# Kernel optimization log

Measured on AMD Instinct MI355X. Metric: run time of the kernel, lower is better.

Reference implementation:

```python
import jax, jax.numpy as jnp
import numpy as np

MASK_SIZE = 28

def _box_iou(a, b):
    # a: [P,4], b: [G,4] in (x1,y1,x2,y2) -> [P,G] IoU (torchvision box_iou semantics)
    area_a = (a[:, 2] - a[:, 0]) * (a[:, 3] - a[:, 1])
    area_b = (b[:, 2] - b[:, 0]) * (b[:, 3] - b[:, 1])
    lt = jnp.maximum(a[:, None, :2], b[None, :, :2])
    rb = jnp.minimum(a[:, None, 2:], b[None, :, 2:])
    wh = jnp.clip(rb - lt, 0.0)
    inter = wh[..., 0] * wh[..., 1]
    return inter / (area_a[:, None] + area_b[None, :] - inter)

def _extract_targets(gt_masks, midx, mboxes):
    # Vectorized equivalent of the per-box Python loop in extract_mask_target:
    # clamp int box, crop gt mask, bilinear-resize (align_corners=False) to 28x28.
    G, H, W = gt_masks.shape
    b = mboxes.astype(jnp.int32)  # .int() truncation; boxes are non-negative here
    x1 = jnp.clip(b[:, 0], 0, W - 1)
    y1 = jnp.clip(b[:, 1], 0, H - 1)
    x2 = jnp.maximum(x1 + 1, jnp.minimum(b[:, 2], W))
    y2 = jnp.maximum(y1 + 1, jnp.minimum(b[:, 3], H))
    cw = (x2 - x1).astype(jnp.float32)
    ch = (y2 - y1).astype(jnp.float32)
    grid = jnp.arange(MASK_SIZE, dtype=jnp.float32) + 0.5
    # source coords inside the crop, align_corners=False, clamped to valid range
    sy = jnp.clip(grid[None, :] * ch[:, None] / MASK_SIZE - 0.5, 0.0, ch[:, None] - 1.0)  # [P,M]
    sx = jnp.clip(grid[None, :] * cw[:, None] / MASK_SIZE - 0.5, 0.0, cw[:, None] - 1.0)
    y0 = jnp.floor(sy).astype(jnp.int32)
    x0 = jnp.floor(sx).astype(jnp.int32)
    yp = jnp.minimum(y0 + 1, (y2 - y1)[:, None] - 1)
    xp = jnp.minimum(x0 + 1, (x2 - x1)[:, None] - 1)
    wy = sy - y0.astype(jnp.float32)
    wx = sx - x0.astype(jnp.float32)
    # shift crop-local coords into full-mask coords and gather 4 corners
    Y0 = y1[:, None] + y0; Y1 = y1[:, None] + yp
    X0 = x1[:, None] + x0; X1 = x1[:, None] + xp
    gi = midx[:, None, None]
    t00 = gt_masks[gi, Y0[:, :, None], X0[:, None, :]]  # [P,M,M]
    t01 = gt_masks[gi, Y0[:, :, None], X1[:, None, :]]
    t10 = gt_masks[gi, Y1[:, :, None], X0[:, None, :]]
    t11 = gt_masks[gi, Y1[:, :, None], X1[:, None, :]]
    wyc = wy[:, :, None]; wxc = wx[:, None, :]
    return ((1 - wyc) * (1 - wxc) * t00 + (1 - wyc) * wxc * t01
            + wyc * (1 - wxc) * t10 + wyc * wxc * t11)

def setup_inputs():
    key = jax.random.key(0)
    kp, kg, km, kl = jax.random.split(key, 4)
    P, G, H, W = 512, 200, 520, 704
    def make_boxes(k, n):
        u = jax.random.uniform(k, (n, 4))
        x1 = u[:, 0] * (W - 110.0)
        y1 = u[:, 1] * (H - 110.0)
        bw = 12.0 + u[:, 2] * 90.0
        bh = 12.0 + u[:, 3] * 90.0
        return jnp.stack([x1, y1, x1 + bw, y1 + bh], axis=1)
    proposals = make_boxes(kp, P)
    gt_boxes = make_boxes(kg, G)
    gt_masks = (jax.random.uniform(km, (G, H, W)) > 0.5).astype(jnp.float32)
    gt_labels = jnp.ones((G,), jnp.int32)
    mask_logits = jax.random.normal(kl, (P, 2, MASK_SIZE, MASK_SIZE), jnp.float32)
    return {"mask_logits": mask_logits, "proposals": proposals, "gt_boxes": gt_boxes,
            "gt_masks": gt_masks, "gt_labels": gt_labels}

def reference(mask_logits, proposals, gt_boxes, gt_masks, gt_labels):
    ious = _box_iou(proposals, gt_boxes)                 # [P,G]
    max_ious = ious.max(axis=1)
    midx = ious.argmax(axis=1)
    pos = (max_ious > 0.3).astype(mask_logits.dtype)     # [P]
    targets = _extract_targets(gt_masks, midx, gt_boxes[midx])  # [P,28,28]
    logits = mask_logits[:, 1]                           # class-1 channel, as in source
    # BCE-with-logits: softplus(x) - x*t  (numerically stable)
    bce = jax.nn.softplus(logits) - logits * targets
    num_pos = pos.sum()
    denom = jnp.maximum(num_pos, 1.0) * (MASK_SIZE * MASK_SIZE)
    loss = (bce * pos[:, None, None]).sum() / denom      # mean over positive boxes
    return jnp.where(num_pos > 0, loss, jnp.zeros((), mask_logits.dtype))
```

## Files before the change

kernel.cpp:

```cpp
#include <hip/hip_runtime.h>
#include <math.h>

#define MASK_SIZE 28
#define MASK_PIX (MASK_SIZE * MASK_SIZE)
#define GT_H 520
#define GT_W 704


__global__ void iou_kernel(const float* __restrict__ proposals,
                           const float* __restrict__ gt_boxes,
                           int P, int G,
                           float* __restrict__ wssum,
                           int* __restrict__ wsnpos,
                           int* __restrict__ wsmidx) {
    extern __shared__ float sb[];
    int tid = threadIdx.x;
    for (int i = tid; i < G * 4; i += blockDim.x) sb[i] = gt_boxes[i];
    __shared__ int s_npos;
    if (tid == 0) s_npos = 0;
    __syncthreads();

    int pos = 0;
    if (tid < P) {
        float ax1 = proposals[tid * 4 + 0], ay1 = proposals[tid * 4 + 1];
        float ax2 = proposals[tid * 4 + 2], ay2 = proposals[tid * 4 + 3];
        float area_a = (ax2 - ax1) * (ay2 - ay1);
        float best = -1.0f;
        int bidx = 0;
        for (int j = 0; j < G; ++j) {
            float bx1 = sb[j * 4 + 0], by1 = sb[j * 4 + 1];
            float bx2 = sb[j * 4 + 2], by2 = sb[j * 4 + 3];
            float area_b = (bx2 - bx1) * (by2 - by1);
            float lx = fmaxf(ax1, bx1), ly = fmaxf(ay1, by1);
            float rx = fminf(ax2, bx2), ry = fminf(ay2, by2);
            float w = fmaxf(rx - lx, 0.0f), h = fmaxf(ry - ly, 0.0f);
            float inter = w * h;
            float iou = inter / (area_a + area_b - inter);
            if (iou > best) { best = iou; bidx = j; }
        }
        pos = (best > 0.3f) ? 1 : 0;
        wsmidx[tid] = pos ? bidx : -1;
    }
    unsigned long long m = __ballot(pos);
    if ((tid & 63) == 0) atomicAdd(&s_npos, __popcll(m));
    __syncthreads();
    if (tid == 0) {
        *wssum = 0.0f;
        *wsnpos = s_npos;
    }
}

__global__ void bce_kernel(const float* __restrict__ mask_logits,
                           const float* __restrict__ gt_boxes,
                           const float* __restrict__ gt_masks,
                           const int* __restrict__ wsmidx,
                           float* __restrict__ wssum,
                           int H, int W) {
    int p = blockIdx.x;
    int g = wsmidx[p];
    if (g < 0) return;

    float bx1f = gt_boxes[g * 4 + 0], by1f = gt_boxes[g * 4 + 1];
    float bx2f = gt_boxes[g * 4 + 2], by2f = gt_boxes[g * 4 + 3];
    int b0 = (int)bx1f, b1 = (int)by1f, b2 = (int)bx2f, b3 = (int)by2f;
    int x1 = min(max(b0, 0), W - 1);
    int y1 = min(max(b1, 0), H - 1);
    int x2 = max(x1 + 1, min(b2, W));
    int y2 = max(y1 + 1, min(b3, H));
    float cw = (float)(x2 - x1), ch = (float)(y2 - y1);
    const float* mrow = gt_masks + (size_t)g * H * W;

    float lsum = 0.0f;
    for (int i = threadIdx.x; i < MASK_PIX; i += blockDim.x) {
        int py = i / MASK_SIZE, px = i % MASK_SIZE;
        float sy = fminf(fmaxf(((float)py + 0.5f) * ch / (float)MASK_SIZE - 0.5f, 0.0f), ch - 1.0f);
        float sx = fminf(fmaxf(((float)px + 0.5f) * cw / (float)MASK_SIZE - 0.5f, 0.0f), cw - 1.0f);
        int y0 = (int)floorf(sy);
        int x0 = (int)floorf(sx);
        int yp = min(y0 + 1, (y2 - y1) - 1);
        int xp = min(x0 + 1, (x2 - x1) - 1);
        float wy = sy - (float)y0;
        float wx = sx - (float)x0;
        int Y0 = y1 + y0, Y1 = y1 + yp, X0 = x1 + x0, X1 = x1 + xp;
        float t00 = mrow[Y0 * W + X0];
        float t01 = mrow[Y0 * W + X1];
        float t10 = mrow[Y1 * W + X0];
        float t11 = mrow[Y1 * W + X1];
        float tgt = (1.0f - wy) * (1.0f - wx) * t00 + (1.0f - wy) * wx * t01
                  + wy * (1.0f - wx) * t10 + wy * wx * t11;
        float l = mask_logits[((size_t)p * 2 + 1) * MASK_PIX + i];
        float bce = fmaxf(l, 0.0f) + log1pf(expf(-fabsf(l))) - l * tgt;
        lsum += bce;
    }

    for (int off = 32; off > 0; off >>= 1) lsum += __shfl_down(lsum, off, 64);
    __shared__ float swave[16];
    int wid = threadIdx.x >> 6;
    if ((threadIdx.x & 63) == 0) swave[wid] = lsum;
    __syncthreads();
    if (threadIdx.x == 0) {
        float tot = 0.0f;
        int nw = blockDim.x >> 6;
        for (int w = 0; w < nw; ++w) tot += swave[w];
        atomicAdd(wssum, tot);
    }
}

__global__ void finalize_kernel(const float* __restrict__ wssum,
                                const int* __restrict__ wsnpos,
                                float* __restrict__ out) {
    float s = *wssum;
    int np = *wsnpos;
    float denom = fmaxf((float)np, 1.0f) * (float)MASK_PIX;
    out[0] = (np > 0) ? (s / denom) : 0.0f;
}

extern "C" void kernel_launch(void* const* d_in, const int* in_sizes, int n_in,
                              void* d_out, int out_size, void* d_ws, size_t ws_size,
                              hipStream_t stream) {
    const float* mask_logits = (const float*)d_in[0];
    const float* proposals   = (const float*)d_in[1];
    const float* gt_boxes    = (const float*)d_in[2];
    const float* gt_masks    = (const float*)d_in[3];
    float* out = (float*)d_out;

    int P = in_sizes[1] / 4;
    int G = in_sizes[2] / 4;

    float* wsf = (float*)d_ws;
    int* wsi = (int*)d_ws;
    float* wssum = &wsf[0];
    int* wsnpos = &wsi[1];
    int* wsmidx = &wsi[2];

    iou_kernel<<<1, P, G * 4 * sizeof(float), stream>>>(proposals, gt_boxes, P, G,
                                                        wssum, wsnpos, wsmidx);
    bce_kernel<<<P, 256, 0, stream>>>(mask_logits, gt_boxes, gt_masks, wsmidx, wssum,
                                      GT_H, GT_W);
    finalize_kernel<<<1, 1, 0, stream>>>(wssum, wsnpos, out);
}
```

Before: 354.6 us.

## Fuse IoU matching, BCE, and finalize into one kernel with last-block reduction

```diff
diff --git a/kernel.cpp b/kernel.cpp
--- a/kernel.cpp
+++ b/kernel.cpp
@@ -7,112 +7,115 @@
 #define GT_W 704
 
 
-__global__ void iou_kernel(const float* __restrict__ proposals,
-                           const float* __restrict__ gt_boxes,
-                           int P, int G,
-                           float* __restrict__ wssum,
-                           int* __restrict__ wsnpos,
-                           int* __restrict__ wsmidx) {
-    extern __shared__ float sb[];
-    int tid = threadIdx.x;
-    for (int i = tid; i < G * 4; i += blockDim.x) sb[i] = gt_boxes[i];
-    __shared__ int s_npos;
-    if (tid == 0) s_npos = 0;
+__global__ __launch_bounds__(256) void fused_kernel(
+        const float* __restrict__ mask_logits,
+        const float* __restrict__ proposals,
+        const float* __restrict__ gt_boxes,
+        const float* __restrict__ gt_masks,
+        int G, int H, int W, int nblocks,
+        float* __restrict__ wssum,
+        int* __restrict__ wsnpos,
+        int* __restrict__ wsdone,
+        float* __restrict__ out) {
+    const int p = blockIdx.x;
+    const int tid = threadIdx.x;
+
+    const float ax1 = proposals[p * 4 + 0], ay1 = proposals[p * 4 + 1];
+    const float ax2 = proposals[p * 4 + 2], ay2 = proposals[p * 4 + 3];
+    const float area_a = (ax2 - ax1) * (ay2 - ay1);
+
+    float best = -1.0f;
+    int bidx = 0x7fffffff;
+    for (int j = tid; j < G; j += blockDim.x) {
+        float bx1 = gt_boxes[j * 4 + 0], by1 = gt_boxes[j * 4 + 1];
+        float bx2 = gt_boxes[j * 4 + 2], by2 = gt_boxes[j * 4 + 3];
+        float area_b = (bx2 - bx1) * (by2 - by1);
+        float lx = fmaxf(ax1, bx1), ly = fmaxf(ay1, by1);
+        float rx = fminf(ax2, bx2), ry = fminf(ay2, by2);
+        float w = fmaxf(rx - lx, 0.0f), h = fmaxf(ry - ly, 0.0f);
+        float inter = w * h;
+        float iou = inter / (area_a + area_b - inter);
+        if (iou > best) { best = iou; bidx = j; }
+    }
+    for (int off = 32; off > 0; off >>= 1) {
+        float ob = __shfl_down(best, off, 64);
+        int   oi = __shfl_down(bidx, off, 64);
+        if (ob > best || (ob == best && oi < bidx)) { best = ob; bidx = oi; }
+    }
+    __shared__ float sbest[4];
+    __shared__ int   sbidx[4];
+    const int wid = tid >> 6;
+    if ((tid & 63) == 0) { sbest[wid] = best; sbidx[wid] = bidx; }
     __syncthreads();
-
-    int pos = 0;
-    if (tid < P) {
-        float ax1 = proposals[tid * 4 + 0], ay1 = proposals[tid * 4 + 1];
-        float ax2 = proposals[tid * 4 + 2], ay2 = proposals[tid * 4 + 3];
-        float area_a = (ax2 - ax1) * (ay2 - ay1);
-        float best = -1.0f;
-        int bidx = 0;
-        for (int j = 0; j < G; ++j) {
-            float bx1 = sb[j * 4 + 0], by1 = sb[j * 4 + 1];
-            float bx2 = sb[j * 4 + 2], by2 = sb[j * 4 + 3];
-            float area_b = (bx2 - bx1) * (by2 - by1);
-            float lx = fmaxf(ax1, bx1), ly = fmaxf(ay1, by1);
-            float rx = fminf(ax2, bx2), ry = fminf(ay2, by2);
-            float w = fmaxf(rx - lx, 0.0f), h = fmaxf(ry - ly, 0.0f);
-            float inter = w * h;
-            float iou = inter / (area_a + area_b - inter);
-            if (iou > best) { best = iou; bidx = j; }
+    {
+        best = sbest[0]; bidx = sbidx[0];
+        const int nw = blockDim.x >> 6;
+        for (int w2 = 1; w2 < nw; ++w2) {
+            if (sbest[w2] > best || (sbest[w2] == best && sbidx[w2] < bidx)) {
+                best = sbest[w2]; bidx = sbidx[w2];
+            }
         }
-        pos = (best > 0.3f) ? 1 : 0;
-        wsmidx[tid] = pos ? bidx : -1;
     }
-    unsigned long long m = __ballot(pos);
-    if ((tid & 63) == 0) atomicAdd(&s_npos, __popcll(m));
-    __syncthreads();
-    if (tid == 0) {
-        *wssum = 0.0f;
-        *wsnpos = s_npos;
-    }
-}
-
-__global__ void bce_kernel(const float* __restrict__ mask_logits,
-                           const float* __restrict__ gt_boxes,
-                           const float* __restrict__ gt_masks,
-                           const int* __restrict__ wsmidx,
-                           float* __restrict__ wssum,
-                           int H, int W) {
-    int p = blockIdx.x;
-    int g = wsmidx[p];
-    if (g < 0) return;
-
-    float bx1f = gt_boxes[g * 4 + 0], by1f = gt_boxes[g * 4 + 1];
-    float bx2f = gt_boxes[g * 4 + 2], by2f = gt_boxes[g * 4 + 3];
-    int b0 = (int)bx1f, b1 = (int)by1f, b2 = (int)bx2f, b3 = (int)by2f;
-    int x1 = min(max(b0, 0), W - 1);
-    int y1 = min(max(b1, 0), H - 1);
-    int x2 = max(x1 + 1, min(b2, W));
-    int y2 = max(y1 + 1, min(b3, H));
-    float cw = (float)(x2 - x1), ch = (float)(y2 - y1);
-    const float* mrow = gt_masks + (size_t)g * H * W;
+    const int pos = (best > 0.3f) ? 1 : 0;
 
     float lsum = 0.0f;
-    for (int i = threadIdx.x; i < MASK_PIX; i += blockDim.x) {
-        int py = i / MASK_SIZE, px = i % MASK_SIZE;
-        float sy = fminf(fmaxf(((float)py + 0.5f) * ch / (float)MASK_SIZE - 0.5f, 0.0f), ch - 1.0f);
-        float sx = fminf(fmaxf(((float)px + 0.5f) * cw / (float)MASK_SIZE - 0.5f, 0.0f), cw - 1.0f);
-        int y0 = (int)floorf(sy);
-        int x0 = (int)floorf(sx);
-        int yp = min(y0 + 1, (y2 - y1) - 1);
-        int xp = min(x0 + 1, (x2 - x1) - 1);
-        float wy = sy - (float)y0;
-        float wx = sx - (float)x0;
-        int Y0 = y1 + y0, Y1 = y1 + yp, X0 = x1 + x0, X1 = x1 + xp;
-        float t00 = mrow[Y0 * W + X0];
-        float t01 = mrow[Y0 * W + X1];
-        float t10 = mrow[Y1 * W + X0];
-        float t11 = mrow[Y1 * W + X1];
-        float tgt = (1.0f - wy) * (1.0f - wx) * t00 + (1.0f - wy) * wx * t01
-                  + wy * (1.0f - wx) * t10 + wy * wx * t11;
-        float l = mask_logits[((size_t)p * 2 + 1) * MASK_PIX + i];
-        float bce = fmaxf(l, 0.0f) + log1pf(expf(-fabsf(l))) - l * tgt;
-        lsum += bce;
+    if (pos) {
+        const int g = bidx;
+        float bx1f = gt_boxes[g * 4 + 0], by1f = gt_boxes[g * 4 + 1];
+        float bx2f = gt_boxes[g * 4 + 2], by2f = gt_boxes[g * 4 + 3];
+        int b0 = (int)bx1f, b1 = (int)by1f, b2 = (int)bx2f, b3 = (int)by2f;
+        int x1 = min(max(b0, 0), W - 1);
+        int y1 = min(max(b1, 0), H - 1);
+        int x2 = max(x1 + 1, min(b2, W));
+        int y2 = max(y1 + 1, min(b3, H));
+        float cw = (float)(x2 - x1), ch = (float)(y2 - y1);
+        const float* mrow = gt_masks + (size_t)g * H * W;
+
+        for (int i = tid; i < MASK_PIX; i += blockDim.x) {
+            int py = i / MASK_SIZE, px = i - py * MASK_SIZE;
+            float sy = fminf(fmaxf(((float)py + 0.5f) * ch / (float)MASK_SIZE - 0.5f, 0.0f), ch - 1.0f);
+            float sx = fminf(fmaxf(((float)px + 0.5f) * cw / (float)MASK_SIZE - 0.5f, 0.0f), cw - 1.0f);
+            int y0 = (int)floorf(sy);
+            int x0 = (int)floorf(sx);
+            int yp = min(y0 + 1, (y2 - y1) - 1);
+            int xp = min(x0 + 1, (x2 - x1) - 1);
+            float wy = sy - (float)y0;
+            float wx = sx - (float)x0;
+            int Y0 = y1 + y0, Y1 = y1 + yp, X0 = x1 + x0, X1 = x1 + xp;
+            float t00 = mrow[Y0 * W + X0];
+            float t01 = mrow[Y0 * W + X1];
+            float t10 = mrow[Y1 * W + X0];
+            float t11 = mrow[Y1 * W + X1];
+            float tgt = (1.0f - wy) * (1.0f - wx) * t00 + (1.0f - wy) * wx * t01
+                      + wy * (1.0f - wx) * t10 + wy * wx * t11;
+            float l = mask_logits[((size_t)p * 2 + 1) * MASK_PIX + i];
+            float bce = fmaxf(l, 0.0f) + log1pf(expf(-fabsf(l))) - l * tgt;
+            lsum += bce;
+        }
     }
 
     for (int off = 32; off > 0; off >>= 1) lsum += __shfl_down(lsum, off, 64);
-    __shared__ float swave[16];
-    int wid = threadIdx.x >> 6;
-    if ((threadIdx.x & 63) == 0) swave[wid] = lsum;
+    __shared__ float swave[4];
+    if ((tid & 63) == 0) swave[wid] = lsum;
     __syncthreads();
-    if (threadIdx.x == 0) {
-        float tot = 0.0f;
-        int nw = blockDim.x >> 6;
-        for (int w = 0; w < nw; ++w) tot += swave[w];
-        atomicAdd(wssum, tot);
+
+    if (tid == 0) {
+        if (pos) {
+            float tot = 0.0f;
+            const int nw = blockDim.x >> 6;
+            for (int w2 = 0; w2 < nw; ++w2) tot += swave[w2];
+            atomicAdd(wssum, tot);
+            atomicAdd(wsnpos, 1);
+        }
+        __threadfence();
+        int done = atomicAdd(wsdone, 1);
+        if (done == nblocks - 1) {
+            float s = atomicAdd(wssum, 0.0f);
+            int  np = atomicAdd(wsnpos, 0);
+            float denom = fmaxf((float)np, 1.0f) * (float)MASK_PIX;
+            out[0] = (np > 0) ? (s / denom) : 0.0f;
+        }
     }
-}
-
-__global__ void finalize_kernel(const float* __restrict__ wssum,
-                                const int* __restrict__ wsnpos,
-                                float* __restrict__ out) {
-    float s = *wssum;
-    int np = *wsnpos;
-    float denom = fmaxf((float)np, 1.0f) * (float)MASK_PIX;
-    out[0] = (np > 0) ? (s / denom) : 0.0f;
 }
 
 extern "C" void kernel_launch(void* const* d_in, const int* in_sizes, int n_in,
@@ -129,13 +132,10 @@
 
     float* wsf = (float*)d_ws;
     int* wsi = (int*)d_ws;
-    float* wssum = &wsf[0];
-    int* wsnpos = &wsi[1];
-    int* wsmidx = &wsi[2];
 
-    iou_kernel<<<1, P, G * 4 * sizeof(float), stream>>>(proposals, gt_boxes, P, G,
-                                                        wssum, wsnpos, wsmidx);
-    bce_kernel<<<P, 256, 0, stream>>>(mask_logits, gt_boxes, gt_masks, wsmidx, wssum,
-                                      GT_H, GT_W);
-    finalize_kernel<<<1, 1, 0, stream>>>(wssum, wsnpos, out);
+    hipMemsetAsync(d_ws, 0, 16, stream);
+
+    fused_kernel<<<P, 256, 0, stream>>>(mask_logits, proposals, gt_boxes, gt_masks,
+                                        G, GT_H, GT_W, P,
+                                        &wsf[0], &wsi[1], &wsi[2], out);
 }
```

New measurement: 346.2 us. 2.4% less time.
